# Kernel optimization log

Hardware: AMD Instinct MI355X
Metric: run time of the kernel (lower is better)

## Reference

```python
import jax, jax.numpy as jnp
import numpy as np

HQ, HKV, HD = 32, 8, 64
G = HQ // HKV
SCALE = HD ** -0.5


def _rope(x, offset=0):
    # x: [B, L, H, hd], interleaved-pair rotary as in the torch module
    B, L, H, hd = x.shape
    inv = 1.0 / (10000.0 ** (jnp.arange(0, hd, 2, dtype=jnp.float32) / hd))  # [hd/2]
    pos = jnp.arange(offset, offset + L, dtype=jnp.float32)
    f = pos[:, None] * inv[None, :]                     # [L, hd/2]
    c = jnp.cos(f)[None, :, None, :]
    s = jnp.sin(f)[None, :, None, :]
    x1, x2 = x[..., 0::2], x[..., 1::2]
    out = jnp.stack([x1 * c - x2 * s, x1 * s + x2 * c], axis=-1)  # [B,L,H,hd/2,2]
    return out.reshape(x.shape)


def setup_inputs() -> dict:
    key = jax.random.key(0)
    ks = jax.random.split(key, 5)
    B, L, D = 2, 2048, 2048
    w = 0.02
    return {
        "x": jax.random.normal(ks[0], (B, L, D), dtype=jnp.float32),
        "Wq": jax.random.normal(ks[1], (HQ * HD, D), dtype=jnp.float32) * w,
        "Wk": jax.random.normal(ks[2], (HKV * HD, D), dtype=jnp.float32) * w,
        "Wv": jax.random.normal(ks[3], (HKV * HD, D), dtype=jnp.float32) * w,
        "Wo": jax.random.normal(ks[4], (D, HQ * HD), dtype=jnp.float32) * w,
    }


def reference(x, Wq, Wk, Wv, Wo):
    B, L, D = x.shape
    q = (x @ Wq.T).reshape(B, L, HQ, HD)
    k = (x @ Wk.T).reshape(B, L, HKV, HD)
    v = (x @ Wv.T).reshape(B, L, HKV, HD)
    q = _rope(q)
    k = _rope(k)
    # GQA via broadcasting instead of repeat_interleave:
    # q head i attends kv head i // G -> group axis g
    qh = q.transpose(0, 2, 1, 3).reshape(B, HKV, G, L, HD)  # [B,Hkv,G,L,hd]
    kh = k.transpose(0, 2, 1, 3)                             # [B,Hkv,L,hd]
    vh = v.transpose(0, 2, 1, 3)
    attn = jnp.einsum("bkgqd,bkld->bkgql", qh, kh) * SCALE
    causal = jnp.arange(L)[:, None] >= jnp.arange(L)[None, :]  # kv_len == L
    attn = jnp.where(causal[None, None, None], attn, -jnp.inf)
    p = jax.nn.softmax(attn, axis=-1)
    out = jnp.einsum("bkgql,bkld->bkgqd", p, vh)             # [B,Hkv,G,L,hd]
    out = out.reshape(B, HQ, L, HD).transpose(0, 2, 1, 3).reshape(B, L, HQ * HD)
    return out @ Wo.T
```

## Files before the change

### kernel.cpp

```cpp
#include <hip/hip_runtime.h>
#include <hip/hip_bf16.h>
#include <hip/hip_fp16.h>

typedef unsigned short u16;
typedef __attribute__((ext_vector_type(8))) short     bf16x8;
typedef __attribute__((ext_vector_type(4))) float     f32x4;
typedef __attribute__((ext_vector_type(4))) _Float16  f16x4;
typedef __attribute__((ext_vector_type(8))) _Float16  f16x8;
typedef __attribute__((ext_vector_type(4))) u16       u16x4;

static constexpr int B_ = 2, L_ = 2048, D_ = 2048;
static constexpr int HQ_ = 32, HD_ = 64;
static constexpr int M_ = B_ * L_;
static constexpr int KVD_ = 512;
static constexpr int NQKV_ = D_ + 2 * KVD_;
static constexpr float QSCALE_ = 0.125f * 1.44269504f;

__device__ __forceinline__ u16 f2bf(float x) {
  union { float f; unsigned u; } c; c.f = x;
  unsigned r = c.u + 0x7FFFu + ((c.u >> 16) & 1u);
  return (u16)(r >> 16);
}

__global__ void cvt5_kernel(const float* __restrict__ s0, const float* __restrict__ s1,
                            const float* __restrict__ s2, const float* __restrict__ s3,
                            const float* __restrict__ s4, u16* __restrict__ dst,
                            long p0, long p1, long p2, long p3, long ntot4) {
  long i = (long)blockIdx.x * blockDim.x + threadIdx.x;
  if (i >= ntot4) return;
  const float* src; long lo;
  if (i < p0)      { src = s0; lo = i; }
  else if (i < p1) { src = s1; lo = i - p0; }
  else if (i < p2) { src = s2; lo = i - p1; }
  else if (i < p3) { src = s3; lo = i - p2; }
  else             { src = s4; lo = i - p3; }
  float4 v = ((const float4*)src)[lo];
  u16x4 w;
  w[0] = f2bf(v.x); w[1] = f2bf(v.y); w[2] = f2bf(v.z); w[3] = f2bf(v.w);
  ((u16x4*)dst)[i] = w;
}

__device__ __forceinline__ void gld_lds16(const void* g, void* l) {
  __builtin_amdgcn_global_load_lds((const __attribute__((address_space(1))) void*)g,
                                   (__attribute__((address_space(3))) void*)l, 16, 0, 0);
}

template <int OUTM>
__global__ __launch_bounds__(256) void gemm_bt(const u16* __restrict__ A,
                                               const u16* __restrict__ Bm,
                                               void* __restrict__ C,
                                               int M, int N, int K) {
  __shared__ u16 As[128 * 32];
  __shared__ u16 Bs[128 * 32];
  const int tid  = threadIdx.x;
  const int lane = tid & 63;
  const int wave = tid >> 6;
  const int wr = wave >> 1, wc = wave & 1;
  const int nwg = gridDim.x * gridDim.y;
  const int bid = blockIdx.y * gridDim.x + blockIdx.x;
  const int swz = (bid & 7) * (nwg >> 3) + (bid >> 3);
  const long bm = (long)(swz / gridDim.x) * 128;
  const long bn = (long)(swz % gridDim.x) * 128;

  f32x4 acc[4][4] = {};

  const u16* ag = A + (bm + wave * 32 + (lane >> 2)) * (long)K + (lane & 3) * 8;
  const u16* bg = Bm + (bn + wave * 32 + (lane >> 2)) * (long)K + (lane & 3) * 8;
  u16* asl0 = &As[wave * 1024];
  u16* asl1 = &As[wave * 1024 + 512];
  u16* bsl0 = &Bs[wave * 1024];
  u16* bsl1 = &Bs[wave * 1024 + 512];

  for (int k0 = 0; k0 < K; k0 += 32) {
    __syncthreads();
    gld_lds16(ag + k0, asl0);
    gld_lds16(ag + k0 + 16 * (long)K, asl1);
    gld_lds16(bg + k0, bsl0);
    gld_lds16(bg + k0 + 16 * (long)K, bsl1);
    __syncthreads();
    bf16x8 af[4], bf[4];
    const int kx = (lane >> 4) * 8;
#pragma unroll
    for (int m = 0; m < 4; ++m)
      af[m] = *(const bf16x8*)&As[(wr * 64 + m * 16 + (lane & 15)) * 32 + kx];
#pragma unroll
    for (int n = 0; n < 4; ++n)
      bf[n] = *(const bf16x8*)&Bs[(wc * 64 + n * 16 + (lane & 15)) * 32 + kx];
#pragma unroll
    for (int m = 0; m < 4; ++m)
#pragma unroll
      for (int n = 0; n < 4; ++n)
        acc[m][n] = __builtin_amdgcn_mfma_f32_16x16x32_bf16(af[m], bf[n], acc[m][n], 0, 0, 0);
  }

  const int cw = lane & 15;
  const int rg = (lane >> 4) * 4;
#pragma unroll
  for (int m = 0; m < 4; ++m) {
    const long row0 = bm + wr * 64 + m * 16 + rg;
#pragma unroll
    for (int n = 0; n < 4; ++n) {
      const long col = bn + wc * 64 + n * 16 + cw;
      if (OUTM == 2) {
#pragma unroll
        for (int j = 0; j < 4; ++j)
          ((float*)C)[(row0 + j) * (long)N + col] = acc[m][n][j];
      } else {
        u16* qb = (u16*)C;
        u16* kb = qb + (long)M_ * D_;
        _Float16* vt = (_Float16*)(kb + (long)M_ * KVD_);
        if (bn < D_ + KVD_) {
          const int i2 = (int)(col & 63) >> 1;
          const float inv = __expf(-(float)(2 * i2) * (9.210340372f / 64.f));
          const bool odd = (cw & 1);
#pragma unroll
          for (int j = 0; j < 4; ++j) {
            const float v = acc[m][n][j];
            const float p = __shfl_xor(v, 1);
            const int pos = (int)((row0 + j) & (L_ - 1));
            float sn, cs;
            __sincosf((float)pos * inv, &sn, &cs);
            const float r = odd ? (p * sn + v * cs) : (v * cs - p * sn);
            if (bn < D_) qb[(row0 + j) * (long)D_ + col] = f2bf(r * QSCALE_);
            else         kb[(row0 + j) * (long)KVD_ + (col - D_)] = f2bf(r);
          }
        } else {
          f16x4 w;
#pragma unroll
          for (int j = 0; j < 4; ++j) w[j] = (_Float16)acc[m][n][j];
          const long off3 = (row0 >> 11) * ((long)KVD_ * L_) + (col - D_ - KVD_) * (long)L_ + (row0 & (L_ - 1));
          *(f16x4*)(vt + off3) = w;
        }
      }
    }
  }
}

__device__ __forceinline__ void sm_step(f32x4 (&s)[4], f16x4 (&pb)[4], float& l_run,
                                        int kv0, int qbase, int qq, int kg) {
  if (kv0 + 63 > qbase) {
    const int qrow = qbase + qq;
    const int kb0 = kv0 + 4 * kg;
#pragma unroll
    for (int ks = 0; ks < 4; ++ks)
#pragma unroll
      for (int j = 0; j < 4; ++j)
        s[ks][j] = (kb0 + ks * 16 + j <= qrow) ? s[ks][j] : -INFINITY;
  }
  float ps[4];
#pragma unroll
  for (int ks = 0; ks < 4; ++ks) {
    const float p0 = exp2f(s[ks][0]), p1 = exp2f(s[ks][1]);
    const float p2 = exp2f(s[ks][2]), p3 = exp2f(s[ks][3]);
    pb[ks][0] = (_Float16)p0; pb[ks][1] = (_Float16)p1;
    pb[ks][2] = (_Float16)p2; pb[ks][3] = (_Float16)p3;
    ps[ks] = (p0 + p1) + (p2 + p3);
  }
  l_run += (ps[0] + ps[1]) + (ps[2] + ps[3]);
}

__device__ __forceinline__ void pv_step(const f16x4 (&va)[4][4], const f16x4 (&pb)[4],
                                        f32x4 (&acc)[4]) {
  __builtin_amdgcn_s_setprio(1);
#pragma unroll
  for (int ks = 0; ks < 4; ++ks)
#pragma unroll
    for (int dt = 0; dt < 4; ++dt)
      acc[dt] = __builtin_amdgcn_mfma_f32_16x16x16f16(va[ks][dt], pb[ks], acc[dt], 0, 0, 0);
  __builtin_amdgcn_s_setprio(0);
}

__global__ __launch_bounds__(256) void attn_kernel(const u16* __restrict__ Q,
                                                   const u16* __restrict__ Kb,
                                                   const _Float16* __restrict__ VT,
                                                   u16* __restrict__ O) {
  const int bid = blockIdx.x;
  const int kvh = bid & 7;
  const int idx = bid >> 3;
  const int q4  = idx & 15;
  const int hh  = (idx >> 4) & 3;
  const int b   = idx >> 6;
  const int s4  = idx >> 5;
  int qblk;
  if (s4 == 0)      qblk = q4;
  else if (s4 == 1) qblk = 15 - q4;
  else if (s4 == 2) qblk = (q4 + 8) & 15;
  else              qblk = (7 - q4) & 15;
  const int h = kvh * 4 + hh;

  const int tid = threadIdx.x, lane = tid & 63, wave = tid >> 6;
  const int qq = lane & 15, kg = lane >> 4;

  __shared__ u16      Ks[2][2][64 * 64];
  __shared__ _Float16 Vs[2][2][64 * 64];

  const int q0 = qblk * 128 + wave * 32;
  bf16x8 qf[2][2];
#pragma unroll
  for (int f = 0; f < 2; ++f) {
    const u16* qp = Q + (long)(b * L_ + q0 + f * 16 + qq) * D_ + h * 64 + kg * 8;
    qf[f][0] = *(const bf16x8*)qp;
    qf[f][1] = *(const bf16x8*)(qp + 32);
  }
  f32x4 acc0[4] = {}, acc1[4] = {};
  float l0 = 0.f, l1 = 0.f;
  const int ntiles = qblk + 1;

  const u16*      kbase = Kb + (long)b * L_ * KVD_ + kvh * 64;
  const _Float16* vbase = VT + (long)b * ((long)KVD_ * L_) + (long)(kvh * 64) * L_;

  auto stage = [&](int buf, int t) {
    const long kv0 = (long)t * 128;
#pragma unroll
    for (int v = 0; v < 2; ++v) {
#pragma unroll
      for (int i = 0; i < 2; ++i) {
        const int c   = tid + i * 256;
        const int row = c >> 3;
        const int s16 = (c & 7) ^ (row & 7);
        gld_lds16(kbase + (kv0 + v * 64 + row) * KVD_ + s16 * 8, (u16*)&Ks[buf][v][0] + c * 8);
        gld_lds16(vbase + (long)row * L_ + kv0 + v * 64 + s16 * 8, (_Float16*)&Vs[buf][v][0] + c * 8);
      }
    }
  };

  stage(0, 0);
  __syncthreads();

  for (int t = 0; t < ntiles; ++t) {
    const int buf = t & 1;
    if (t + 1 < ntiles) stage(buf ^ 1, t + 1);

    const int sw = (qq & 7) << 4;
#pragma unroll
    for (int v = 0; v < 2; ++v) {
      const int kv0 = t * 128 + v * 64;
      const char* ksb = (const char*)&Ks[buf][v][0];
      const char* vsb = (const char*)&Vs[buf][v][0];

      bf16x8 kf[4][2];
#pragma unroll
      for (int ks = 0; ks < 4; ++ks) {
        const int rowb = (ks * 16 + qq) * 128;
        kf[ks][0] = *(const bf16x8*)(ksb + rowb + ((kg * 16) ^ sw));
        kf[ks][1] = *(const bf16x8*)(ksb + rowb + ((kg * 16 + 64) ^ sw));
      }
      f16x4 va[4][4];
#pragma unroll
      for (int ks = 0; ks < 4; ++ks)
#pragma unroll
        for (int dt = 0; dt < 4; ++dt)
          va[ks][dt] = *(const f16x4*)(vsb + (dt * 16 + qq) * 128 + ((ks * 32 + kg * 8) ^ sw));

      f32x4 s[4];
      f16x4 pb[4];
#pragma unroll
      for (int ks = 0; ks < 4; ++ks) {
        f32x4 z = {};
        z = __builtin_amdgcn_mfma_f32_16x16x32_bf16(kf[ks][0], qf[0][0], z, 0, 0, 0);
        z = __builtin_amdgcn_mfma_f32_16x16x32_bf16(kf[ks][1], qf[0][1], z, 0, 0, 0);
        s[ks] = z;
      }
      sm_step(s, pb, l0, kv0, q0, qq, kg);
      pv_step(va, pb, acc0);
#pragma unroll
      for (int ks = 0; ks < 4; ++ks) {
        f32x4 z = {};
        z = __builtin_amdgcn_mfma_f32_16x16x32_bf16(kf[ks][0], qf[1][0], z, 0, 0, 0);
        z = __builtin_amdgcn_mfma_f32_16x16x32_bf16(kf[ks][1], qf[1][1], z, 0, 0, 0);
        s[ks] = z;
      }
      sm_step(s, pb, l1, kv0, q0 + 16, qq, kg);
      pv_step(va, pb, acc1);
    }

    __syncthreads();
  }

#pragma unroll
  for (int f = 0; f < 2; ++f) {
    const f32x4* accw = f ? acc1 : acc0;
    float lr = f ? l1 : l0;
    lr += __shfl_xor(lr, 16);
    lr += __shfl_xor(lr, 32);
    const float inv_l = 1.f / lr;
    const long row = (long)(b * L_ + q0 + f * 16 + qq);
#pragma unroll
    for (int dt = 0; dt < 4; ++dt) {
      u16x4 w2;
#pragma unroll
      for (int j = 0; j < 4; ++j) w2[j] = f2bf(accw[dt][j] * inv_l);
      *(u16x4*)(O + row * D_ + h * 64 + dt * 16 + 4 * kg) = w2;
    }
  }
}

extern "C" void kernel_launch(void* const* d_in, const int* in_sizes, int n_in,
                              void* d_out, int out_size, void* d_ws, size_t ws_size,
                              hipStream_t stream) {
  const float* x  = (const float*)d_in[0];
  const float* Wq = (const float*)d_in[1];
  const float* Wk = (const float*)d_in[2];
  const float* Wv = (const float*)d_in[3];
  const float* Wo = (const float*)d_in[4];
  float* out = (float*)d_out;
  char* ws = (char*)d_ws;
  size_t off = 0;
  auto alloc = [&](size_t bytes) -> void* {
    void* p = ws + off; off += (bytes + 255) & ~(size_t)255; return p;
  };
  u16* x_bf  = (u16*)alloc((size_t)M_ * D_ * 2);
  u16* wq_bf = (u16*)alloc((size_t)D_ * D_ * 2);
  u16* wk_bf = (u16*)alloc((size_t)KVD_ * D_ * 2);
  u16* wv_bf = (u16*)alloc((size_t)KVD_ * D_ * 2);
  u16* wo_bf = (u16*)alloc((size_t)D_ * D_ * 2);
  u16* qb = (u16*)alloc((size_t)M_ * D_ * 2);
  u16* kb = (u16*)alloc((size_t)M_ * KVD_ * 2);
  _Float16* vt = (_Float16*)alloc((size_t)M_ * KVD_ * 2);
  u16* ao = (u16*)alloc((size_t)M_ * D_ * 2);

  {
    const long q0 = (long)M_ * D_ / 4;
    const long q1 = q0 + (long)D_ * D_ / 4;
    const long q2 = q1 + (long)KVD_ * D_ / 4;
    const long q3 = q2 + (long)KVD_ * D_ / 4;
    const long qt = q3 + (long)D_ * D_ / 4;
    cvt5_kernel<<<(int)((qt + 255) / 256), 256, 0, stream>>>(x, Wq, Wk, Wv, Wo, x_bf,
                                                             q0, q1, q2, q3, qt);
  }

  dim3 blk(256);
  gemm_bt<4><<<dim3(NQKV_ / 128, M_ / 128), blk, 0, stream>>>(x_bf, wq_bf, qb, M_, NQKV_, D_);

  attn_kernel<<<dim3(1024), dim3(256), 0, stream>>>(qb, kb, vt, ao);

  gemm_bt<2><<<dim3(D_ / 128, M_ / 128), blk, 0, stream>>>(ao, wo_bf, (void*)out, M_, D_, D_);
}
```

Before: 244.5 us.

## Deepen attention KV pipeline to 4 buffers with 64-row tiles and partial waitcnt

Replaces the double-buffered 128-row KV staging in the attention kernel with a four-slot ring of 64-row tiles, prefetching two tiles ahead. It uses explicit s_waitcnt vmcnt(4) and a raw s_barrier in place of __syncthreads, so the current tile's loads are waited on while the next tile's stay in flight. The aim is to hide global-to-LDS latency and cut barrier stalls. In exchange there are twice as many loop iterations and barriers, and correctness now depends on the hand-counted vmcnt matching the number of outstanding loads.

```diff
diff --git a/kernel.cpp b/kernel.cpp
--- a/kernel.cpp
+++ b/kernel.cpp
@@ -191,8 +191,8 @@
   const int tid = threadIdx.x, lane = tid & 63, wave = tid >> 6;
   const int qq = lane & 15, kg = lane >> 4;
 
-  __shared__ u16      Ks[2][2][64 * 64];
-  __shared__ _Float16 Vs[2][2][64 * 64];
+  __shared__ u16      Ks[4][64 * 64];
+  __shared__ _Float16 Vs[4][64 * 64];
 
   const int q0 = qblk * 128 + wave * 32;
   bf16x8 qf[2][2];
@@ -204,77 +204,80 @@
   }
   f32x4 acc0[4] = {}, acc1[4] = {};
   float l0 = 0.f, l1 = 0.f;
-  const int ntiles = qblk + 1;
+  const int ntiles = 2 * qblk + 2;
 
   const u16*      kbase = Kb + (long)b * L_ * KVD_ + kvh * 64;
   const _Float16* vbase = VT + (long)b * ((long)KVD_ * L_) + (long)(kvh * 64) * L_;
 
   auto stage = [&](int buf, int t) {
-    const long kv0 = (long)t * 128;
-#pragma unroll
-    for (int v = 0; v < 2; ++v) {
-#pragma unroll
-      for (int i = 0; i < 2; ++i) {
-        const int c   = tid + i * 256;
-        const int row = c >> 3;
-        const int s16 = (c & 7) ^ (row & 7);
-        gld_lds16(kbase + (kv0 + v * 64 + row) * KVD_ + s16 * 8, (u16*)&Ks[buf][v][0] + c * 8);
-        gld_lds16(vbase + (long)row * L_ + kv0 + v * 64 + s16 * 8, (_Float16*)&Vs[buf][v][0] + c * 8);
-      }
+    const long kv0 = (long)t * 64;
+#pragma unroll
+    for (int i = 0; i < 2; ++i) {
+      const int c   = tid + i * 256;
+      const int row = c >> 3;
+      const int s16 = (c & 7) ^ (row & 7);
+      gld_lds16(kbase + (kv0 + row) * KVD_ + s16 * 8, (u16*)&Ks[buf][0] + c * 8);
+      gld_lds16(vbase + (long)row * L_ + kv0 + s16 * 8, (_Float16*)&Vs[buf][0] + c * 8);
     }
   };
 
   stage(0, 0);
-  __syncthreads();
+  if (1 < ntiles) stage(1, 1);
+  if (1 < ntiles) { asm volatile("s_waitcnt vmcnt(4)" ::: "memory"); }
+  else            { asm volatile("s_waitcnt vmcnt(0)" ::: "memory"); }
+  __builtin_amdgcn_s_barrier();
+  __builtin_amdgcn_sched_barrier(0);
 
   for (int t = 0; t < ntiles; ++t) {
-    const int buf = t & 1;
-    if (t + 1 < ntiles) stage(buf ^ 1, t + 1);
-
+    const int buf = t & 3;
+    const bool more2 = (t + 2) < ntiles;
+    if (more2) stage((t + 2) & 3, t + 2);
+
+    const int kv0 = t * 64;
     const int sw = (qq & 7) << 4;
-#pragma unroll
-    for (int v = 0; v < 2; ++v) {
-      const int kv0 = t * 128 + v * 64;
-      const char* ksb = (const char*)&Ks[buf][v][0];
-      const char* vsb = (const char*)&Vs[buf][v][0];
-
-      bf16x8 kf[4][2];
-#pragma unroll
-      for (int ks = 0; ks < 4; ++ks) {
-        const int rowb = (ks * 16 + qq) * 128;
-        kf[ks][0] = *(const bf16x8*)(ksb + rowb + ((kg * 16) ^ sw));
-        kf[ks][1] = *(const bf16x8*)(ksb + rowb + ((kg * 16 + 64) ^ sw));
-      }
-      f16x4 va[4][4];
-#pragma unroll
-      for (int ks = 0; ks < 4; ++ks)
-#pragma unroll
-        for (int dt = 0; dt < 4; ++dt)
-          va[ks][dt] = *(const f16x4*)(vsb + (dt * 16 + qq) * 128 + ((ks * 32 + kg * 8) ^ sw));
-
-      f32x4 s[4];
-      f16x4 pb[4];
-#pragma unroll
-      for (int ks = 0; ks < 4; ++ks) {
-        f32x4 z = {};
-        z = __builtin_amdgcn_mfma_f32_16x16x32_bf16(kf[ks][0], qf[0][0], z, 0, 0, 0);
-        z = __builtin_amdgcn_mfma_f32_16x16x32_bf16(kf[ks][1], qf[0][1], z, 0, 0, 0);
-        s[ks] = z;
-      }
-      sm_step(s, pb, l0, kv0, q0, qq, kg);
-      pv_step(va, pb, acc0);
-#pragma unroll
-      for (int ks = 0; ks < 4; ++ks) {
-        f32x4 z = {};
-        z = __builtin_amdgcn_mfma_f32_16x16x32_bf16(kf[ks][0], qf[1][0], z, 0, 0, 0);
-        z = __builtin_amdgcn_mfma_f32_16x16x32_bf16(kf[ks][1], qf[1][1], z, 0, 0, 0);
-        s[ks] = z;
-      }
-      sm_step(s, pb, l1, kv0, q0 + 16, qq, kg);
-      pv_step(va, pb, acc1);
-    }
-
-    __syncthreads();
+    const char* ksb = (const char*)&Ks[buf][0];
+    const char* vsb = (const char*)&Vs[buf][0];
+
+    bf16x8 kf[4][2];
+#pragma unroll
+    for (int ks = 0; ks < 4; ++ks) {
+      const int rowb = (ks * 16 + qq) * 128;
+      kf[ks][0] = *(const bf16x8*)(ksb + rowb + ((kg * 16) ^ sw));
+      kf[ks][1] = *(const bf16x8*)(ksb + rowb + ((kg * 16 + 64) ^ sw));
+    }
+    f16x4 va[4][4];
+#pragma unroll
+    for (int ks = 0; ks < 4; ++ks)
+#pragma unroll
+      for (int dt = 0; dt < 4; ++dt)
+        va[ks][dt] = *(const f16x4*)(vsb + (dt * 16 + qq) * 128 + ((ks * 32 + kg * 8) ^ sw));
+
+    f32x4 s[4];
+    f16x4 pb[4];
+#pragma unroll
+    for (int ks = 0; ks < 4; ++ks) {
+      f32x4 z = {};
+      z = __builtin_amdgcn_mfma_f32_16x16x32_bf16(kf[ks][0], qf[0][0], z, 0, 0, 0);
+      z = __builtin_amdgcn_mfma_f32_16x16x32_bf16(kf[ks][1], qf[0][1], z, 0, 0, 0);
+      s[ks] = z;
+    }
+    sm_step(s, pb, l0, kv0, q0, qq, kg);
+    pv_step(va, pb, acc0);
+#pragma unroll
+    for (int ks = 0; ks < 4; ++ks) {
+      f32x4 z = {};
+      z = __builtin_amdgcn_mfma_f32_16x16x32_bf16(kf[ks][0], qf[1][0], z, 0, 0, 0);
+      z = __builtin_amdgcn_mfma_f32_16x16x32_bf16(kf[ks][1], qf[1][1], z, 0, 0, 0);
+      s[ks] = z;
+    }
+    sm_step(s, pb, l1, kv0, q0 + 16, qq, kg);
+    pv_step(va, pb, acc1);
+
+    __builtin_amdgcn_sched_barrier(0);
+    if (more2) { asm volatile("s_waitcnt vmcnt(4)" ::: "memory"); }
+    else       { asm volatile("s_waitcnt vmcnt(0)" ::: "memory"); }
+    __builtin_amdgcn_s_barrier();
+    __builtin_amdgcn_sched_barrier(0);
   }
 
 #pragma unroll
```

After: 256.0 us. 1.05x slower.

## Double GEMM K-tile to 64 with XOR-swizzled LDS layout

Applied to the files above, without the earlier changes.

The bf16 GEMM now stages a 128x64 K-slab per iteration instead of 128x32, using a cooperative load loop with an XOR chunk swizzle. Fragment reads apply the matching swizzle to avoid LDS bank conflicts, and two MFMA k-substeps run per barrier pair. This halves the synchronisation count per K and is meant to improve LDS read throughput, at the cost of doubling LDS usage per block, which may reduce occupancy.

```diff
diff --git a/kernel.cpp b/kernel.cpp
--- a/kernel.cpp
+++ b/kernel.cpp
@@ -50,12 +50,13 @@
                                                const u16* __restrict__ Bm,
                                                void* __restrict__ C,
                                                int M, int N, int K) {
-  __shared__ u16 As[128 * 32];
-  __shared__ u16 Bs[128 * 32];
+  __shared__ u16 As[128 * 64];
+  __shared__ u16 Bs[128 * 64];
   const int tid  = threadIdx.x;
   const int lane = tid & 63;
   const int wave = tid >> 6;
   const int wr = wave >> 1, wc = wave & 1;
+  const int qq = lane & 15, kg = lane >> 4;
   const int nwg = gridDim.x * gridDim.y;
   const int bid = blockIdx.y * gridDim.x + blockIdx.x;
   const int swz = (bid & 7) * (nwg >> 3) + (bid >> 3);
@@ -64,33 +65,35 @@
 
   f32x4 acc[4][4] = {};
 
-  const u16* ag = A + (bm + wave * 32 + (lane >> 2)) * (long)K + (lane & 3) * 8;
-  const u16* bg = Bm + (bn + wave * 32 + (lane >> 2)) * (long)K + (lane & 3) * 8;
-  u16* asl0 = &As[wave * 1024];
-  u16* asl1 = &As[wave * 1024 + 512];
-  u16* bsl0 = &Bs[wave * 1024];
-  u16* bsl1 = &Bs[wave * 1024 + 512];
-
-  for (int k0 = 0; k0 < K; k0 += 32) {
+  for (int k0 = 0; k0 < K; k0 += 64) {
     __syncthreads();
-    gld_lds16(ag + k0, asl0);
-    gld_lds16(ag + k0 + 16 * (long)K, asl1);
-    gld_lds16(bg + k0, bsl0);
-    gld_lds16(bg + k0 + 16 * (long)K, bsl1);
+#pragma unroll
+    for (int i = 0; i < 4; ++i) {
+      const int ch  = tid + i * 256;
+      const int row = ch >> 3;
+      const int s8  = ((ch & 7) ^ (row & 7)) * 8;
+      gld_lds16(A  + (bm + row) * (long)K + k0 + s8, &As[ch * 8]);
+      gld_lds16(Bm + (bn + row) * (long)K + k0 + s8, &Bs[ch * 8]);
+    }
     __syncthreads();
-    bf16x8 af[4], bf[4];
-    const int kx = (lane >> 4) * 8;
-#pragma unroll
-    for (int m = 0; m < 4; ++m)
-      af[m] = *(const bf16x8*)&As[(wr * 64 + m * 16 + (lane & 15)) * 32 + kx];
-#pragma unroll
-    for (int n = 0; n < 4; ++n)
-      bf[n] = *(const bf16x8*)&Bs[(wc * 64 + n * 16 + (lane & 15)) * 32 + kx];
-#pragma unroll
-    for (int m = 0; m < 4; ++m)
+
+    const int sw = (qq & 7) << 4;
+#pragma unroll
+    for (int ks2 = 0; ks2 < 2; ++ks2) {
+      const int kb = ks2 * 64 + kg * 16;
+      bf16x8 af[4], bf[4];
+#pragma unroll
+      for (int m = 0; m < 4; ++m)
+        af[m] = *(const bf16x8*)((const char*)As + (wr * 64 + m * 16 + qq) * 128 + (kb ^ sw));
 #pragma unroll
       for (int n = 0; n < 4; ++n)
-        acc[m][n] = __builtin_amdgcn_mfma_f32_16x16x32_bf16(af[m], bf[n], acc[m][n], 0, 0, 0);
+        bf[n] = *(const bf16x8*)((const char*)Bs + (wc * 64 + n * 16 + qq) * 128 + (kb ^ sw));
+#pragma unroll
+      for (int m = 0; m < 4; ++m)
+#pragma unroll
+        for (int n = 0; n < 4; ++n)
+          acc[m][n] = __builtin_amdgcn_mfma_f32_16x16x32_bf16(af[m], bf[n], acc[m][n], 0, 0, 0);
+    }
   }
 
   const int cw = lane & 15;
@@ -107,8 +110,8 @@
           ((float*)C)[(row0 + j) * (long)N + col] = acc[m][n][j];
       } else {
         u16* qb = (u16*)C;
-        u16* kb = qb + (long)M_ * D_;
-        _Float16* vt = (_Float16*)(kb + (long)M_ * KVD_);
+        u16* kb2 = qb + (long)M_ * D_;
+        _Float16* vt = (_Float16*)(kb2 + (long)M_ * KVD_);
         if (bn < D_ + KVD_) {
           const int i2 = (int)(col & 63) >> 1;
           const float inv = __expf(-(float)(2 * i2) * (9.210340372f / 64.f));
@@ -122,7 +125,7 @@
             __sincosf((float)pos * inv, &sn, &cs);
             const float r = odd ? (p * sn + v * cs) : (v * cs - p * sn);
             if (bn < D_) qb[(row0 + j) * (long)D_ + col] = f2bf(r * QSCALE_);
-            else         kb[(row0 + j) * (long)KVD_ + (col - D_)] = f2bf(r);
+            else         kb2[(row0 + j) * (long)KVD_ + (col - D_)] = f2bf(r);
           }
         } else {
           f16x4 w;
```

Measured after the change: 231.9 us. 1.05x faster.
